# Kernel tuning notes

Measured on AMD Instinct MI355X. Metric: run time of the kernel, lower is better.

Reference implementation:

```python
import jax, jax.numpy as jnp
import numpy as np

B = 16384      # batch
T = 14         # number of embedding tables
L = 100000     # rows per table (table has L+1 rows due to the +1 offset)
E = 16         # em_size
H = 50         # user click history length


def setup_inputs() -> dict:
    key = jax.random.key(0)
    ks = jax.random.split(key, 10)
    sparse_features = jax.random.randint(ks[0], (B, T), 0, L, dtype=jnp.int32)
    dense_features = jax.random.normal(ks[1], (B, 1), dtype=jnp.float32)
    user_click_history = jax.random.randint(ks[2], (B, H), 0, L, dtype=jnp.int32)
    # stacked EmbeddingBag weights: [T, L+1, E]
    W = jax.random.normal(ks[3], (T, L + 1, E), dtype=jnp.float32) * 0.01
    fc1_w = jax.random.normal(ks[4], (200, 241), dtype=jnp.float32) / np.sqrt(241).astype(np.float32)
    fc1_b = jnp.zeros((200,), jnp.float32)
    fc2_w = jax.random.normal(ks[5], (80, 200), dtype=jnp.float32) / np.sqrt(200).astype(np.float32)
    fc2_b = jnp.zeros((80,), jnp.float32)
    fc3_w = jax.random.normal(ks[6], (2, 80), dtype=jnp.float32) / np.sqrt(80).astype(np.float32)
    fc3_b = jnp.zeros((2,), jnp.float32)
    return dict(sparse_features=sparse_features, dense_features=dense_features,
                user_click_history=user_click_history, W=W,
                fc1_w=fc1_w, fc1_b=fc1_b, fc2_w=fc2_w, fc2_b=fc2_b,
                fc3_w=fc3_w, fc3_b=fc3_b)


def reference(sparse_features, dense_features, user_click_history, W,
              fc1_w, fc1_b, fc2_w, fc2_b, fc3_w, fc3_b):
    # Per-table single-index EmbeddingBag(sum) == plain lookup. Batched gather
    # across all T tables at once: [B, T, E]
    embs = W[jnp.arange(T)[None, :], sparse_features + 1]
    embs = embs.reshape(embs.shape[0], T * E)  # [B, T*E]
    # tables[0].weight row 0 is zeroed before the history lookup (padding row).
    W0 = W[0].at[0].set(0.0)
    hist = W0[user_click_history + 1].sum(axis=1)  # [B, E] EmbeddingBag sum
    x = jnp.concatenate([embs, hist, dense_features], axis=1)  # [B, 241]
    x = jax.nn.relu(x @ fc1_w.T + fc1_b)
    x = jax.nn.relu(x @ fc2_w.T + fc2_b)
    return x @ fc3_w.T + fc3_b  # [B, 2]
```

## Files before the change

kernel.cpp:

```cpp
#include <hip/hip_runtime.h>


using u16 = unsigned short;
typedef __attribute__((ext_vector_type(8))) short short8v;
typedef __attribute__((ext_vector_type(4))) short short4v;
typedef __attribute__((ext_vector_type(4))) float floatx4;

constexpr int W1_ELEMS = 13 * 8 * 64 * 8;
constexpr int W2_ELEMS = 5 * 7 * 64 * 8;

__device__ __forceinline__ u16 f2bf(float f) {
  unsigned u = __float_as_uint(f);
  unsigned r = (u + 0x7fffu + ((u >> 16) & 1u)) >> 16;
  return (u16)r;
}
__device__ __forceinline__ float bf2f(u16 h) {
  return __uint_as_float(((unsigned)h) << 16);
}

__global__ void build_frags(const float* __restrict__ w1, const float* __restrict__ w2,
                            u16* __restrict__ w1h, u16* __restrict__ w2h) {
  int tid = blockIdx.x * blockDim.x + threadIdx.x;
  if (tid < 13 * 8 * 64) {
    int l = tid & 63;
    int g = tid >> 6;
    int kt = g & 7, nt = g >> 3;
    int n = nt * 16 + (l & 15);
    int kb = kt * 32 + (l >> 4) * 8;
    short8v h8;
#pragma unroll
    for (int e = 0; e < 8; ++e) {
      int k = kb + e;
      float v = (n < 200 && k < 241) ? w1[n * 241 + k] : 0.f;
      h8[e] = (short)f2bf(v);
    }
    *(short8v*)&w1h[tid * 8] = h8;
  } else if (tid < 13 * 8 * 64 + 5 * 7 * 64) {
    int t2 = tid - 13 * 8 * 64;
    int l = t2 & 63;
    int g = t2 >> 6;
    int kt = g % 7, nt = g / 7;
    int n = nt * 16 + (l & 15);
    int kb = kt * 32 + (l >> 4) * 8;
    short8v h8;
#pragma unroll
    for (int e = 0; e < 8; ++e) {
      int k = kb + e;
      float v = (k < 200) ? w2[n * 200 + k] : 0.f;
      h8[e] = (short)f2bf(v);
    }
    *(short8v*)&w2h[t2 * 8] = h8;
  }
}

__global__ __launch_bounds__(256, 4) void fused_kernel(
    const int* __restrict__ sf, const float* __restrict__ dense,
    const int* __restrict__ hist, const float* __restrict__ W,
    const u16* __restrict__ w1h, const u16* __restrict__ w2h,
    const float* __restrict__ b1, const float* __restrict__ b2,
    const float* __restrict__ w3, const float* __restrict__ b3,
    float* __restrict__ out) {
  __shared__ u16 A1h[8 * 64 * 8], A1l[8 * 64 * 8];
  __shared__ u16 A2h[7 * 64 * 8], A2l[7 * 64 * 8];
  __shared__ float o2[16 * 84];

  const int tid = threadIdx.x;
  const int l = tid & 63;
  const int wv = tid >> 6;
  const int row0 = blockIdx.x * 16;
  short8v z8 = {0, 0, 0, 0, 0, 0, 0, 0};

  const int ntbase = (wv == 0) ? 0 : 4 + 3 * (wv - 1);
  const int ntcnt = (wv == 0) ? 4 : 3;

  short8v bhr[2][4];
#pragma unroll
  for (int kk = 0; kk < 2; ++kk)
#pragma unroll
    for (int i = 0; i < 4; ++i)
      bhr[kk][i] = (i < ntcnt) ? *(const short8v*)&w1h[(((ntbase + i) * 8 + kk) * 64 + l) * 8]
                               : z8;

#pragma unroll
  for (int it = 0; it < 4; ++it) {
    int g = tid + it * 256;
    if (g < 896) {
      int q = g & 3, rt = g >> 2;
      int r = rt & 15, t = rt >> 4;
      int idx = sf[(row0 + r) * 14 + t] + 1;
      const float* p = W + ((size_t)t * 100001 + (size_t)idx) * 16 + q * 4;
      int k0 = t * 16 + q * 4;
      int kt = k0 >> 5, kg = (k0 >> 3) & 3, e0 = k0 & 7;
      short4v h4, l4;
#pragma unroll
      for (int d = 0; d < 4; ++d) {
        float v = p[d];
        u16 hi = f2bf(v);
        h4[d] = (short)hi;
        l4[d] = (short)f2bf(v - bf2f(hi));
      }
      int base = (kt * 64 + kg * 16 + r) * 8 + e0;
      *(short4v*)&A1h[base] = h4;
      *(short4v*)&A1l[base] = l4;
    }
  }

  {
    int r = tid >> 4, rem = tid & 15, q = rem & 3, s = rem >> 2;
    const int* hp = hist + (row0 + r) * 50;
    const float* Wq = W + q * 4;
    float a0 = 0.f, a1 = 0.f, a2 = 0.f, a3 = 0.f;
#pragma unroll
    for (int hh = 0; hh < 12; ++hh) {
      int idx = hp[s + hh * 4] + 1;
      const float* p = Wq + (size_t)idx * 16;
      a0 += p[0];
      a1 += p[1];
      a2 += p[2];
      a3 += p[3];
    }
    if (s < 2) {
      int idx = hp[48 + s] + 1;
      const float* p = Wq + (size_t)idx * 16;
      a0 += p[0];
      a1 += p[1];
      a2 += p[2];
      a3 += p[3];
    }
    a0 += __shfl_xor(a0, 4);
    a1 += __shfl_xor(a1, 4);
    a2 += __shfl_xor(a2, 4);
    a3 += __shfl_xor(a3, 4);
    a0 += __shfl_xor(a0, 8);
    a1 += __shfl_xor(a1, 8);
    a2 += __shfl_xor(a2, 8);
    a3 += __shfl_xor(a3, 8);
    if (s == 0) {
      float vals[4] = {a0, a1, a2, a3};
      short4v h4, l4;
#pragma unroll
      for (int d = 0; d < 4; ++d) {
        u16 hi = f2bf(vals[d]);
        h4[d] = (short)hi;
        l4[d] = (short)f2bf(vals[d] - bf2f(hi));
      }
      int base = (7 * 64 + (q >> 1) * 16 + r) * 8 + ((q * 4) & 7);
      *(short4v*)&A1h[base] = h4;
      *(short4v*)&A1l[base] = l4;
      if (q == 0) {
        float dv = dense[row0 + r];
        u16 dh = f2bf(dv), dl = f2bf(dv - bf2f(dh));
        short8v dh8 = z8, dl8 = z8;
        dh8[0] = (short)dh;
        dl8[0] = (short)dl;
        *(short8v*)&A1h[(7 * 64 + 32 + r) * 8] = dh8;
        *(short8v*)&A1l[(7 * 64 + 32 + r) * 8] = dl8;
        *(short8v*)&A1h[(7 * 64 + 48 + r) * 8] = z8;
        *(short8v*)&A1l[(7 * 64 + 48 + r) * 8] = z8;
      }
    }
  }
  __syncthreads();

  floatx4 acc[4];
#pragma unroll
  for (int i = 0; i < 4; ++i) acc[i] = (floatx4){0.f, 0.f, 0.f, 0.f};

#pragma unroll
  for (int kt = 0; kt < 8; ++kt) {
    short8v ah = *(const short8v*)&A1h[(kt * 64 + l) * 8];
    short8v al = *(const short8v*)&A1l[(kt * 64 + l) * 8];
#pragma unroll
    for (int i = 0; i < 4; ++i) {
      if (i < ntcnt) {
        short8v cb = bhr[kt & 1][i];
        if (kt < 6) bhr[kt & 1][i] = *(const short8v*)&w1h[(((ntbase + i) * 8 + kt + 2) * 64 + l) * 8];
        acc[i] = __builtin_amdgcn_mfma_f32_16x16x32_bf16(ah, cb, acc[i], 0, 0, 0);
        acc[i] = __builtin_amdgcn_mfma_f32_16x16x32_bf16(al, cb, acc[i], 0, 0, 0);
      }
    }
  }

  const int ntA = wv;
  short8v bra[2], brb[2];
  bra[0] = *(const short8v*)&w2h[((ntA * 7 + 0) * 64 + l) * 8];
  bra[1] = *(const short8v*)&w2h[((ntA * 7 + 1) * 64 + l) * 8];
  if (wv == 0) {
    brb[0] = *(const short8v*)&w2h[((4 * 7 + 0) * 64 + l) * 8];
    brb[1] = *(const short8v*)&w2h[((4 * 7 + 1) * 64 + l) * 8];
  } else {
    brb[0] = z8;
    brb[1] = z8;
  }

#pragma unroll
  for (int i = 0; i < 4; ++i) {
    if (i < ntcnt) {
      int n = (ntbase + i) * 16 + (l & 15);
      float bias = (n < 200) ? b1[n] : 0.f;
#pragma unroll
      for (int g = 0; g < 4; ++g) {
        float v = (n < 200) ? fmaxf(acc[i][g] + bias, 0.f) : 0.f;
        int m = (l >> 4) * 4 + g;
        u16 hi = f2bf(v), lo = f2bf(v - bf2f(hi));
        int kt2 = n >> 5, kg2 = (n >> 3) & 3, e = n & 7;
        int pos = (kt2 * 64 + kg2 * 16 + m) * 8 + e;
        A2h[pos] = hi;
        A2l[pos] = lo;
      }
    }
  }
  if (wv == 1 && l < 32) {
    *(short8v*)&A2h[(6 * 64 + 32 + l) * 8] = z8;
    *(short8v*)&A2l[(6 * 64 + 32 + l) * 8] = z8;
  }
  __syncthreads();

  floatx4 acca = (floatx4){0.f, 0.f, 0.f, 0.f};
  floatx4 accb = (floatx4){0.f, 0.f, 0.f, 0.f};
#pragma unroll
  for (int kt = 0; kt < 7; ++kt) {
    short8v ah = *(const short8v*)&A2h[(kt * 64 + l) * 8];
    short8v al = *(const short8v*)&A2l[(kt * 64 + l) * 8];
    short8v ca = bra[kt & 1];
    if (kt < 5) bra[kt & 1] = *(const short8v*)&w2h[((ntA * 7 + kt + 2) * 64 + l) * 8];
    acca = __builtin_amdgcn_mfma_f32_16x16x32_bf16(ah, ca, acca, 0, 0, 0);
    acca = __builtin_amdgcn_mfma_f32_16x16x32_bf16(al, ca, acca, 0, 0, 0);
    if (wv == 0) {
      short8v cb = brb[kt & 1];
      if (kt < 5) brb[kt & 1] = *(const short8v*)&w2h[((4 * 7 + kt + 2) * 64 + l) * 8];
      accb = __builtin_amdgcn_mfma_f32_16x16x32_bf16(ah, cb, accb, 0, 0, 0);
      accb = __builtin_amdgcn_mfma_f32_16x16x32_bf16(al, cb, accb, 0, 0, 0);
    }
  }

  {
    int n = ntA * 16 + (l & 15);
    float bias = b2[n];
#pragma unroll
    for (int g = 0; g < 4; ++g) {
      int r = (l >> 4) * 4 + g;
      o2[r * 84 + n] = fmaxf(acca[g] + bias, 0.f);
    }
    if (wv == 0) {
      int n2 = 64 + (l & 15);
      float bias2 = b2[n2];
#pragma unroll
      for (int g = 0; g < 4; ++g) {
        int r = (l >> 4) * 4 + g;
        o2[r * 84 + n2] = fmaxf(accb[g] + bias2, 0.f);
      }
    }
  }
  __syncthreads();

  if (tid < 32) {
    int r = tid >> 1, o = tid & 1;
    float a = b3[o];
    const float* orow = &o2[r * 84];
    const float* wrow = &w3[o * 80];
#pragma unroll
    for (int j = 0; j < 80; j += 4) {
      floatx4 xv = *(const floatx4*)&orow[j];
      floatx4 wv4 = *(const floatx4*)&wrow[j];
      a += xv[0] * wv4[0] + xv[1] * wv4[1] + xv[2] * wv4[2] + xv[3] * wv4[3];
    }
    out[(row0 + r) * 2 + o] = a;
  }
}

extern "C" void kernel_launch(void* const* d_in, const int* in_sizes, int n_in,
                              void* d_out, int out_size, void* d_ws, size_t ws_size,
                              hipStream_t stream) {
  const int* sf = (const int*)d_in[0];
  const float* dense = (const float*)d_in[1];
  const int* hist = (const int*)d_in[2];
  const float* W = (const float*)d_in[3];
  const float* w1 = (const float*)d_in[4];
  const float* b1 = (const float*)d_in[5];
  const float* w2 = (const float*)d_in[6];
  const float* b2 = (const float*)d_in[7];
  const float* w3 = (const float*)d_in[8];
  const float* b3 = (const float*)d_in[9];
  float* out = (float*)d_out;

  u16* w1h = (u16*)d_ws;
  u16* w2h = w1h + W1_ELEMS;

  build_frags<<<dim3(35), dim3(256), 0, stream>>>(w1, w2, w1h, w2h);
  fused_kernel<<<dim3(1024), dim3(256), 0, stream>>>(sf, dense, hist, W, w1h, w2h,
                                                     b1, b2, w3, b3, out);
}
```

Before: 31.08 us.

## Convert table 0 to bf16 for history gather and drop low-part MFMAs for embeddings

Adds a precompute pass that converts all of table 0 to bf16 each call. The history EmbeddingBag then gathers half-size bf16 rows, using 8 lanes per row with 16-byte loads. The 14 sparse embeddings are now rounded to a single bf16 and keep no low-part residual, so the hi/lo split MFMA runs only for the history/dense tile. This halves the MFMA count for layer 1 and shrinks shared memory. The trade-offs are extra per-call conversion traffic over a 6.4MB table and reduced precision in both embedding paths. Note that table 0 row 0 is not zeroed, though the before code had the same issue.

```diff
diff --git a/kernel.cpp b/kernel.cpp
--- a/kernel.cpp
+++ b/kernel.cpp
@@ -8,6 +8,8 @@
 
 constexpr int W1_ELEMS = 13 * 8 * 64 * 8;
 constexpr int W2_ELEMS = 5 * 7 * 64 * 8;
+constexpr int W0_ROWS = 100001;
+constexpr int W0_ELEMS = W0_ROWS * 16;
 
 __device__ __forceinline__ u16 f2bf(float f) {
   unsigned u = __float_as_uint(f);
@@ -18,49 +20,73 @@
   return __uint_as_float(((unsigned)h) << 16);
 }
 
-__global__ void build_frags(const float* __restrict__ w1, const float* __restrict__ w2,
-                            u16* __restrict__ w1h, u16* __restrict__ w2h) {
-  int tid = blockIdx.x * blockDim.x + threadIdx.x;
-  if (tid < 13 * 8 * 64) {
-    int l = tid & 63;
-    int g = tid >> 6;
-    int kt = g & 7, nt = g >> 3;
-    int n = nt * 16 + (l & 15);
-    int kb = kt * 32 + (l >> 4) * 8;
-    short8v h8;
-#pragma unroll
-    for (int e = 0; e < 8; ++e) {
-      int k = kb + e;
-      float v = (n < 200 && k < 241) ? w1[n * 241 + k] : 0.f;
-      h8[e] = (short)f2bf(v);
-    }
-    *(short8v*)&w1h[tid * 8] = h8;
-  } else if (tid < 13 * 8 * 64 + 5 * 7 * 64) {
-    int t2 = tid - 13 * 8 * 64;
-    int l = t2 & 63;
-    int g = t2 >> 6;
-    int kt = g % 7, nt = g / 7;
-    int n = nt * 16 + (l & 15);
-    int kb = kt * 32 + (l >> 4) * 8;
-    short8v h8;
-#pragma unroll
-    for (int e = 0; e < 8; ++e) {
-      int k = kb + e;
-      float v = (k < 200) ? w2[n * 200 + k] : 0.f;
-      h8[e] = (short)f2bf(v);
-    }
-    *(short8v*)&w2h[t2 * 8] = h8;
+__global__ void precompute(const float* __restrict__ w1, const float* __restrict__ w2,
+                           const float* __restrict__ W,
+                           u16* __restrict__ w1h, u16* __restrict__ w2h,
+                           u16* __restrict__ w0b) {
+  int b = blockIdx.x;
+  if (b < 35) {
+    int tid = b * 256 + threadIdx.x;
+    if (tid < 13 * 8 * 64) {
+      int l = tid & 63;
+      int g = tid >> 6;
+      int kt = g & 7, nt = g >> 3;
+      int n = nt * 16 + (l & 15);
+      int kb = kt * 32 + (l >> 4) * 8;
+      short8v h8;
+#pragma unroll
+      for (int e = 0; e < 8; ++e) {
+        int k = kb + e;
+        float v = (n < 200 && k < 241) ? w1[n * 241 + k] : 0.f;
+        h8[e] = (short)f2bf(v);
+      }
+      *(short8v*)&w1h[tid * 8] = h8;
+    } else if (tid < 13 * 8 * 64 + 5 * 7 * 64) {
+      int t2 = tid - 13 * 8 * 64;
+      int l = t2 & 63;
+      int g = t2 >> 6;
+      int kt = g % 7, nt = g / 7;
+      int n = nt * 16 + (l & 15);
+      int kb = kt * 32 + (l >> 4) * 8;
+      short8v h8;
+#pragma unroll
+      for (int e = 0; e < 8; ++e) {
+        int k = kb + e;
+        float v = (k < 200) ? w2[n * 200 + k] : 0.f;
+        h8[e] = (short)f2bf(v);
+      }
+      *(short8v*)&w2h[t2 * 8] = h8;
+    }
+  } else {
+    int t = (b - 35) * 256 + threadIdx.x;
+    int base = t * 8;
+    if (base < W0_ELEMS) {
+      floatx4 f0 = *(const floatx4*)(W + base);
+      floatx4 f1 = *(const floatx4*)(W + base + 4);
+      short8v o;
+      o[0] = (short)f2bf(f0[0]);
+      o[1] = (short)f2bf(f0[1]);
+      o[2] = (short)f2bf(f0[2]);
+      o[3] = (short)f2bf(f0[3]);
+      o[4] = (short)f2bf(f1[0]);
+      o[5] = (short)f2bf(f1[1]);
+      o[6] = (short)f2bf(f1[2]);
+      o[7] = (short)f2bf(f1[3]);
+      *(short8v*)(w0b + base) = o;
+    }
   }
 }
 
 __global__ __launch_bounds__(256, 4) void fused_kernel(
     const int* __restrict__ sf, const float* __restrict__ dense,
     const int* __restrict__ hist, const float* __restrict__ W,
+    const u16* __restrict__ w0b,
     const u16* __restrict__ w1h, const u16* __restrict__ w2h,
     const float* __restrict__ b1, const float* __restrict__ b2,
     const float* __restrict__ w3, const float* __restrict__ b3,
     float* __restrict__ out) {
-  __shared__ u16 A1h[8 * 64 * 8], A1l[8 * 64 * 8];
+  __shared__ u16 A1h[8 * 64 * 8];
+  __shared__ u16 A1l7[64 * 8];
   __shared__ u16 A2h[7 * 64 * 8], A2l[7 * 64 * 8];
   __shared__ float o2[16 * 84];
 
@@ -88,65 +114,50 @@
       int q = g & 3, rt = g >> 2;
       int r = rt & 15, t = rt >> 4;
       int idx = sf[(row0 + r) * 14 + t] + 1;
-      const float* p = W + ((size_t)t * 100001 + (size_t)idx) * 16 + q * 4;
+      const floatx4 v4 = *(const floatx4*)(W + ((size_t)t * 100001 + (size_t)idx) * 16 + q * 4);
       int k0 = t * 16 + q * 4;
       int kt = k0 >> 5, kg = (k0 >> 3) & 3, e0 = k0 & 7;
-      short4v h4, l4;
-#pragma unroll
-      for (int d = 0; d < 4; ++d) {
-        float v = p[d];
-        u16 hi = f2bf(v);
-        h4[d] = (short)hi;
-        l4[d] = (short)f2bf(v - bf2f(hi));
-      }
-      int base = (kt * 64 + kg * 16 + r) * 8 + e0;
-      *(short4v*)&A1h[base] = h4;
-      *(short4v*)&A1l[base] = l4;
+      short4v h4;
+#pragma unroll
+      for (int d = 0; d < 4; ++d) h4[d] = (short)f2bf(v4[d]);
+      *(short4v*)&A1h[(kt * 64 + kg * 16 + r) * 8 + e0] = h4;
     }
   }
 
   {
-    int r = tid >> 4, rem = tid & 15, q = rem & 3, s = rem >> 2;
+    int r = tid >> 4, rem = tid & 15, q = rem & 1, s = rem >> 1;
     const int* hp = hist + (row0 + r) * 50;
-    const float* Wq = W + q * 4;
-    float a0 = 0.f, a1 = 0.f, a2 = 0.f, a3 = 0.f;
-#pragma unroll
-    for (int hh = 0; hh < 12; ++hh) {
-      int idx = hp[s + hh * 4] + 1;
-      const float* p = Wq + (size_t)idx * 16;
-      a0 += p[0];
-      a1 += p[1];
-      a2 += p[2];
-      a3 += p[3];
+    const u16* Wq = w0b + q * 8;
+    float a[8] = {0.f, 0.f, 0.f, 0.f, 0.f, 0.f, 0.f, 0.f};
+#pragma unroll
+    for (int hh = 0; hh < 6; ++hh) {
+      int idx = hp[s + hh * 8] + 1;
+      short8v v = *(const short8v*)(Wq + (size_t)idx * 16);
+#pragma unroll
+      for (int d = 0; d < 8; ++d) a[d] += bf2f((u16)v[d]);
     }
     if (s < 2) {
       int idx = hp[48 + s] + 1;
-      const float* p = Wq + (size_t)idx * 16;
-      a0 += p[0];
-      a1 += p[1];
-      a2 += p[2];
-      a3 += p[3];
-    }
-    a0 += __shfl_xor(a0, 4);
-    a1 += __shfl_xor(a1, 4);
-    a2 += __shfl_xor(a2, 4);
-    a3 += __shfl_xor(a3, 4);
-    a0 += __shfl_xor(a0, 8);
-    a1 += __shfl_xor(a1, 8);
-    a2 += __shfl_xor(a2, 8);
-    a3 += __shfl_xor(a3, 8);
+      short8v v = *(const short8v*)(Wq + (size_t)idx * 16);
+#pragma unroll
+      for (int d = 0; d < 8; ++d) a[d] += bf2f((u16)v[d]);
+    }
+#pragma unroll
+    for (int d = 0; d < 8; ++d) {
+      a[d] += __shfl_xor(a[d], 2);
+      a[d] += __shfl_xor(a[d], 4);
+      a[d] += __shfl_xor(a[d], 8);
+    }
     if (s == 0) {
-      float vals[4] = {a0, a1, a2, a3};
-      short4v h4, l4;
-#pragma unroll
-      for (int d = 0; d < 4; ++d) {
-        u16 hi = f2bf(vals[d]);
-        h4[d] = (short)hi;
-        l4[d] = (short)f2bf(vals[d] - bf2f(hi));
-      }
-      int base = (7 * 64 + (q >> 1) * 16 + r) * 8 + ((q * 4) & 7);
-      *(short4v*)&A1h[base] = h4;
-      *(short4v*)&A1l[base] = l4;
+      short8v h8, l8;
+#pragma unroll
+      for (int d = 0; d < 8; ++d) {
+        u16 hi = f2bf(a[d]);
+        h8[d] = (short)hi;
+        l8[d] = (short)f2bf(a[d] - bf2f(hi));
+      }
+      *(short8v*)&A1h[(7 * 64 + q * 16 + r) * 8] = h8;
+      *(short8v*)&A1l7[(q * 16 + r) * 8] = l8;
       if (q == 0) {
         float dv = dense[row0 + r];
         u16 dh = f2bf(dv), dl = f2bf(dv - bf2f(dh));
@@ -154,9 +165,9 @@
         dh8[0] = (short)dh;
         dl8[0] = (short)dl;
         *(short8v*)&A1h[(7 * 64 + 32 + r) * 8] = dh8;
-        *(short8v*)&A1l[(7 * 64 + 32 + r) * 8] = dl8;
+        *(short8v*)&A1l7[(32 + r) * 8] = dl8;
         *(short8v*)&A1h[(7 * 64 + 48 + r) * 8] = z8;
-        *(short8v*)&A1l[(7 * 64 + 48 + r) * 8] = z8;
+        *(short8v*)&A1l7[(48 + r) * 8] = z8;
       }
     }
   }
@@ -169,14 +180,15 @@
 #pragma unroll
   for (int kt = 0; kt < 8; ++kt) {
     short8v ah = *(const short8v*)&A1h[(kt * 64 + l) * 8];
-    short8v al = *(const short8v*)&A1l[(kt * 64 + l) * 8];
+    short8v al7;
+    if (kt == 7) al7 = *(const short8v*)&A1l7[l * 8];
 #pragma unroll
     for (int i = 0; i < 4; ++i) {
       if (i < ntcnt) {
         short8v cb = bhr[kt & 1][i];
         if (kt < 6) bhr[kt & 1][i] = *(const short8v*)&w1h[(((ntbase + i) * 8 + kt + 2) * 64 + l) * 8];
         acc[i] = __builtin_amdgcn_mfma_f32_16x16x32_bf16(ah, cb, acc[i], 0, 0, 0);
-        acc[i] = __builtin_amdgcn_mfma_f32_16x16x32_bf16(al, cb, acc[i], 0, 0, 0);
+        if (kt == 7) acc[i] = __builtin_amdgcn_mfma_f32_16x16x32_bf16(al7, cb, acc[i], 0, 0, 0);
       }
     }
   }
@@ -286,8 +298,10 @@
 
   u16* w1h = (u16*)d_ws;
   u16* w2h = w1h + W1_ELEMS;
-
-  build_frags<<<dim3(35), dim3(256), 0, stream>>>(w1, w2, w1h, w2h);
-  fused_kernel<<<dim3(1024), dim3(256), 0, stream>>>(sf, dense, hist, W, w1h, w2h,
+  u16* w0b = w2h + W2_ELEMS;
+
+  int conv_blocks = (W0_ELEMS / 8 + 255) / 256;
+  precompute<<<dim3(35 + conv_blocks), dim3(256), 0, stream>>>(w1, w2, W, w1h, w2h, w0b);
+  fused_kernel<<<dim3(1024), dim3(256), 0, stream>>>(sf, dense, hist, W, w0b, w1h, w2h,
                                                      b1, b2, w3, b3, out);
 }
```

Result: faster. 30.28 us (-2.6%).

## Split gathers into a prep kernel and run MLP on 64-row tiles

Applied to the files above, without the earlier changes.

The embedding gathers and history sums move into a separate prep kernel that writes MFMA-ready bf16 fragments to workspace, merged with the weight-fragment build. The MLP kernel then handles 64 rows per block instead of 16, so each weight fragment loaded from global is reused across four row subtiles. The table embeddings now use a single bf16 (hi only) instead of the hi/lo split, which halves the first-layer MFMAs but lowers precision. The cost is an extra global round trip for the activations and far fewer MLP blocks (256), which may leave CUs underused.

```diff
diff --git a/kernel.cpp b/kernel.cpp
--- a/kernel.cpp
+++ b/kernel.cpp
@@ -8,6 +8,8 @@
 
 constexpr int W1_ELEMS = 13 * 8 * 64 * 8;
 constexpr int W2_ELEMS = 5 * 7 * 64 * 8;
+constexpr int EF_ELEMS = 1024 * 7 * 64 * 8;
+constexpr int HS_ELEMS = 1024 * 1024;
 
 __device__ __forceinline__ u16 f2bf(float f) {
   unsigned u = __float_as_uint(f);
@@ -18,102 +20,72 @@
   return __uint_as_float(((unsigned)h) << 16);
 }
 
-__global__ void build_frags(const float* __restrict__ w1, const float* __restrict__ w2,
-                            u16* __restrict__ w1h, u16* __restrict__ w2h) {
-  int tid = blockIdx.x * blockDim.x + threadIdx.x;
-  if (tid < 13 * 8 * 64) {
-    int l = tid & 63;
-    int g = tid >> 6;
-    int kt = g & 7, nt = g >> 3;
-    int n = nt * 16 + (l & 15);
-    int kb = kt * 32 + (l >> 4) * 8;
-    short8v h8;
-#pragma unroll
-    for (int e = 0; e < 8; ++e) {
-      int k = kb + e;
-      float v = (n < 200 && k < 241) ? w1[n * 241 + k] : 0.f;
-      h8[e] = (short)f2bf(v);
-    }
-    *(short8v*)&w1h[tid * 8] = h8;
-  } else if (tid < 13 * 8 * 64 + 5 * 7 * 64) {
-    int t2 = tid - 13 * 8 * 64;
-    int l = t2 & 63;
-    int g = t2 >> 6;
-    int kt = g % 7, nt = g / 7;
-    int n = nt * 16 + (l & 15);
-    int kb = kt * 32 + (l >> 4) * 8;
-    short8v h8;
-#pragma unroll
-    for (int e = 0; e < 8; ++e) {
-      int k = kb + e;
-      float v = (k < 200) ? w2[n * 200 + k] : 0.f;
-      h8[e] = (short)f2bf(v);
-    }
-    *(short8v*)&w2h[t2 * 8] = h8;
-  }
-}
-
-__global__ __launch_bounds__(256, 4) void fused_kernel(
-    const int* __restrict__ sf, const float* __restrict__ dense,
-    const int* __restrict__ hist, const float* __restrict__ W,
-    const u16* __restrict__ w1h, const u16* __restrict__ w2h,
-    const float* __restrict__ b1, const float* __restrict__ b2,
-    const float* __restrict__ w3, const float* __restrict__ b3,
-    float* __restrict__ out) {
-  __shared__ u16 A1h[8 * 64 * 8], A1l[8 * 64 * 8];
-  __shared__ u16 A2h[7 * 64 * 8], A2l[7 * 64 * 8];
-  __shared__ float o2[16 * 84];
-
-  const int tid = threadIdx.x;
-  const int l = tid & 63;
-  const int wv = tid >> 6;
-  const int row0 = blockIdx.x * 16;
+__global__ __launch_bounds__(256) void prep_kernel(
+    const float* __restrict__ w1, const float* __restrict__ w2,
+    const float* __restrict__ W, const int* __restrict__ sf,
+    const int* __restrict__ hist, const float* __restrict__ dense,
+    u16* __restrict__ w1h, u16* __restrict__ w2h,
+    u16* __restrict__ ef, u16* __restrict__ hs) {
+  const int b = blockIdx.x;
+  const int tix = threadIdx.x;
   short8v z8 = {0, 0, 0, 0, 0, 0, 0, 0};
 
-  const int ntbase = (wv == 0) ? 0 : 4 + 3 * (wv - 1);
-  const int ntcnt = (wv == 0) ? 4 : 3;
-
-  short8v bhr[2][4];
-#pragma unroll
-  for (int kk = 0; kk < 2; ++kk)
-#pragma unroll
-    for (int i = 0; i < 4; ++i)
-      bhr[kk][i] = (i < ntcnt) ? *(const short8v*)&w1h[(((ntbase + i) * 8 + kk) * 64 + l) * 8]
-                               : z8;
-
-#pragma unroll
-  for (int it = 0; it < 4; ++it) {
-    int g = tid + it * 256;
-    if (g < 896) {
-      int q = g & 3, rt = g >> 2;
-      int r = rt & 15, t = rt >> 4;
-      int idx = sf[(row0 + r) * 14 + t] + 1;
-      const float* p = W + ((size_t)t * 100001 + (size_t)idx) * 16 + q * 4;
-      int k0 = t * 16 + q * 4;
-      int kt = k0 >> 5, kg = (k0 >> 3) & 3, e0 = k0 & 7;
-      short4v h4, l4;
-#pragma unroll
-      for (int d = 0; d < 4; ++d) {
-        float v = p[d];
-        u16 hi = f2bf(v);
-        h4[d] = (short)hi;
-        l4[d] = (short)f2bf(v - bf2f(hi));
-      }
-      int base = (kt * 64 + kg * 16 + r) * 8 + e0;
-      *(short4v*)&A1h[base] = h4;
-      *(short4v*)&A1l[base] = l4;
-    }
-  }
-
-  {
-    int r = tid >> 4, rem = tid & 15, q = rem & 3, s = rem >> 2;
+  if (b < 35) {
+    int tid = b * 256 + tix;
+    if (tid < 13 * 8 * 64) {
+      int l = tid & 63;
+      int g = tid >> 6;
+      int kt = g & 7, nt = g >> 3;
+      int n = nt * 16 + (l & 15);
+      int kb = kt * 32 + (l >> 4) * 8;
+      short8v h8;
+#pragma unroll
+      for (int e = 0; e < 8; ++e) {
+        int k = kb + e;
+        float v = (n < 200 && k < 241) ? w1[n * 241 + k] : 0.f;
+        h8[e] = (short)f2bf(v);
+      }
+      *(short8v*)&w1h[tid * 8] = h8;
+    } else if (tid < 13 * 8 * 64 + 5 * 7 * 64) {
+      int t2 = tid - 13 * 8 * 64;
+      int l = t2 & 63;
+      int g = t2 >> 6;
+      int kt = g % 7, nt = g / 7;
+      int n = nt * 16 + (l & 15);
+      int kb = kt * 32 + (l >> 4) * 8;
+      short8v h8;
+#pragma unroll
+      for (int e = 0; e < 8; ++e) {
+        int k = kb + e;
+        float v = (k < 200) ? w2[n * 200 + k] : 0.f;
+        h8[e] = (short)f2bf(v);
+      }
+      *(short8v*)&w2h[t2 * 8] = h8;
+    }
+  } else if (b < 3619) {
+    int g = (b - 35) * 256 + tix;
+    int t = g >> 16;
+    int bb = (g >> 2) & 16383;
+    int q = g & 3;
+    int idx = sf[bb * 14 + t] + 1;
+    floatx4 v4 = *(const floatx4*)(W + ((size_t)t * 100001 + (size_t)idx) * 16 + q * 4);
+    short4v h4;
+#pragma unroll
+    for (int d = 0; d < 4; ++d) h4[d] = (short)f2bf(v4[d]);
+    int k0 = t * 16 + q * 4;
+    int kt = k0 >> 5, kg = (k0 >> 3) & 3, e0 = k0 & 7;
+    int tile = bb >> 4, r = bb & 15;
+    *(short4v*)&ef[((tile * 7 + kt) * 64 + kg * 16 + r) * 8 + e0] = h4;
+  } else {
+    int tile = b - 3619;
+    int row0 = tile * 16;
+    int r = tix >> 4, rem = tix & 15, q = rem & 3, s = rem >> 2;
     const int* hp = hist + (row0 + r) * 50;
-    const float* Wq = W + q * 4;
     float a0 = 0.f, a1 = 0.f, a2 = 0.f, a3 = 0.f;
 #pragma unroll
     for (int hh = 0; hh < 12; ++hh) {
       int idx = hp[s + hh * 4] + 1;
-      const float* p = Wq + (size_t)idx * 16;
+      floatx4 p = *(const floatx4*)(W + (size_t)idx * 16 + q * 4);
       a0 += p[0];
       a1 += p[1];
       a2 += p[2];
@@ -121,7 +93,7 @@
     }
     if (s < 2) {
       int idx = hp[48 + s] + 1;
-      const float* p = Wq + (size_t)idx * 16;
+      floatx4 p = *(const floatx4*)(W + (size_t)idx * 16 + q * 4);
       a0 += p[0];
       a1 += p[1];
       a2 += p[2];
@@ -144,93 +116,156 @@
         h4[d] = (short)hi;
         l4[d] = (short)f2bf(vals[d] - bf2f(hi));
       }
-      int base = (7 * 64 + (q >> 1) * 16 + r) * 8 + ((q * 4) & 7);
-      *(short4v*)&A1h[base] = h4;
-      *(short4v*)&A1l[base] = l4;
+      u16* ht = hs + (size_t)tile * 1024;
+      int base = ((q >> 1) * 16 + r) * 8 + ((q * 4) & 7);
+      *(short4v*)&ht[base] = h4;
+      *(short4v*)&ht[512 + base] = l4;
       if (q == 0) {
         float dv = dense[row0 + r];
         u16 dh = f2bf(dv), dl = f2bf(dv - bf2f(dh));
         short8v dh8 = z8, dl8 = z8;
         dh8[0] = (short)dh;
         dl8[0] = (short)dl;
-        *(short8v*)&A1h[(7 * 64 + 32 + r) * 8] = dh8;
-        *(short8v*)&A1l[(7 * 64 + 32 + r) * 8] = dl8;
-        *(short8v*)&A1h[(7 * 64 + 48 + r) * 8] = z8;
-        *(short8v*)&A1l[(7 * 64 + 48 + r) * 8] = z8;
-      }
-    }
-  }
-  __syncthreads();
-
-  floatx4 acc[4];
-#pragma unroll
-  for (int i = 0; i < 4; ++i) acc[i] = (floatx4){0.f, 0.f, 0.f, 0.f};
+        *(short8v*)&ht[(32 + r) * 8] = dh8;
+        *(short8v*)&ht[512 + (32 + r) * 8] = dl8;
+        *(short8v*)&ht[(48 + r) * 8] = z8;
+        *(short8v*)&ht[512 + (48 + r) * 8] = z8;
+      }
+    }
+  }
+}
+
+__global__ __launch_bounds__(256, 1) void mlp_kernel(
+    const u16* __restrict__ ef, const u16* __restrict__ hs,
+    const u16* __restrict__ w1h, const u16* __restrict__ w2h,
+    const float* __restrict__ b1, const float* __restrict__ b2,
+    const float* __restrict__ w3, const float* __restrict__ b3,
+    float* __restrict__ out) {
+  __shared__ u16 A2h[4 * 7 * 64 * 8], A2l[4 * 7 * 64 * 8];
+  __shared__ float o2[64 * 84];
+
+  const int tid = threadIdx.x;
+  const int l = tid & 63;
+  const int wv = tid >> 6;
+  const int blk = blockIdx.x;
+  const int row0 = blk * 64;
+  short8v z8 = {0, 0, 0, 0, 0, 0, 0, 0};
+  const int ntbase = (wv == 0) ? 0 : 4 + 3 * (wv - 1);
+  const int ntcnt = (wv == 0) ? 4 : 3;
+
+  short8v a7h[4], a7l[4];
+#pragma unroll
+  for (int sub = 0; sub < 4; ++sub) {
+    const u16* ht = hs + (size_t)(blk * 4 + sub) * 1024;
+    a7h[sub] = *(const short8v*)&ht[l * 8];
+    a7l[sub] = *(const short8v*)&ht[512 + l * 8];
+  }
+  short8v ga[2][4];
+#pragma unroll
+  for (int kk = 0; kk < 2; ++kk)
+#pragma unroll
+    for (int sub = 0; sub < 4; ++sub)
+      ga[kk][sub] = *(const short8v*)&ef[(((blk * 4 + sub) * 7 + kk) * 64 + l) * 8];
+  short8v bhr[2][4];
+#pragma unroll
+  for (int kk = 0; kk < 2; ++kk)
+#pragma unroll
+    for (int i = 0; i < 4; ++i)
+      bhr[kk][i] = (i < ntcnt) ? *(const short8v*)&w1h[(((ntbase + i) * 8 + kk) * 64 + l) * 8]
+                               : z8;
+
+  floatx4 acc[4][4];
+#pragma unroll
+  for (int i = 0; i < 4; ++i)
+#pragma unroll
+    for (int sub = 0; sub < 4; ++sub) acc[i][sub] = (floatx4){0.f, 0.f, 0.f, 0.f};
 
 #pragma unroll
   for (int kt = 0; kt < 8; ++kt) {
-    short8v ah = *(const short8v*)&A1h[(kt * 64 + l) * 8];
-    short8v al = *(const short8v*)&A1l[(kt * 64 + l) * 8];
+    const int cur = kt & 1;
+    short8v a_[4];
+#pragma unroll
+    for (int sub = 0; sub < 4; ++sub) a_[sub] = (kt < 7) ? ga[cur][sub] : a7h[sub];
+    if (kt < 5) {
+#pragma unroll
+      for (int sub = 0; sub < 4; ++sub)
+        ga[cur][sub] = *(const short8v*)&ef[(((blk * 4 + sub) * 7 + kt + 2) * 64 + l) * 8];
+    }
 #pragma unroll
     for (int i = 0; i < 4; ++i) {
       if (i < ntcnt) {
-        short8v cb = bhr[kt & 1][i];
-        if (kt < 6) bhr[kt & 1][i] = *(const short8v*)&w1h[(((ntbase + i) * 8 + kt + 2) * 64 + l) * 8];
-        acc[i] = __builtin_amdgcn_mfma_f32_16x16x32_bf16(ah, cb, acc[i], 0, 0, 0);
-        acc[i] = __builtin_amdgcn_mfma_f32_16x16x32_bf16(al, cb, acc[i], 0, 0, 0);
+        short8v cb = bhr[cur][i];
+        if (kt < 6)
+          bhr[cur][i] = *(const short8v*)&w1h[(((ntbase + i) * 8 + kt + 2) * 64 + l) * 8];
+#pragma unroll
+        for (int sub = 0; sub < 4; ++sub) {
+          acc[i][sub] = __builtin_amdgcn_mfma_f32_16x16x32_bf16(a_[sub], cb, acc[i][sub], 0, 0, 0);
+          if (kt == 7)
+            acc[i][sub] = __builtin_amdgcn_mfma_f32_16x16x32_bf16(a7l[sub], cb, acc[i][sub], 0, 0, 0);
+        }
       }
     }
   }
 
   const int ntA = wv;
+  const bool dual = (wv == 1);
   short8v bra[2], brb[2];
   bra[0] = *(const short8v*)&w2h[((ntA * 7 + 0) * 64 + l) * 8];
   bra[1] = *(const short8v*)&w2h[((ntA * 7 + 1) * 64 + l) * 8];
-  if (wv == 0) {
-    brb[0] = *(const short8v*)&w2h[((4 * 7 + 0) * 64 + l) * 8];
-    brb[1] = *(const short8v*)&w2h[((4 * 7 + 1) * 64 + l) * 8];
-  } else {
-    brb[0] = z8;
-    brb[1] = z8;
-  }
+  brb[0] = dual ? *(const short8v*)&w2h[((4 * 7 + 0) * 64 + l) * 8] : z8;
+  brb[1] = dual ? *(const short8v*)&w2h[((4 * 7 + 1) * 64 + l) * 8] : z8;
 
 #pragma unroll
   for (int i = 0; i < 4; ++i) {
     if (i < ntcnt) {
       int n = (ntbase + i) * 16 + (l & 15);
       float bias = (n < 200) ? b1[n] : 0.f;
-#pragma unroll
-      for (int g = 0; g < 4; ++g) {
-        float v = (n < 200) ? fmaxf(acc[i][g] + bias, 0.f) : 0.f;
-        int m = (l >> 4) * 4 + g;
-        u16 hi = f2bf(v), lo = f2bf(v - bf2f(hi));
-        int kt2 = n >> 5, kg2 = (n >> 3) & 3, e = n & 7;
-        int pos = (kt2 * 64 + kg2 * 16 + m) * 8 + e;
-        A2h[pos] = hi;
-        A2l[pos] = lo;
+      int kt2 = n >> 5, kg2 = (n >> 3) & 3, e = n & 7;
+#pragma unroll
+      for (int sub = 0; sub < 4; ++sub) {
+#pragma unroll
+        for (int g = 0; g < 4; ++g) {
+          float v = (n < 200) ? fmaxf(acc[i][sub][g] + bias, 0.f) : 0.f;
+          int m = (l >> 4) * 4 + g;
+          u16 hi = f2bf(v), lo = f2bf(v - bf2f(hi));
+          int pos = ((sub * 7 + kt2) * 64 + kg2 * 16 + m) * 8 + e;
+          A2h[pos] = hi;
+          A2l[pos] = lo;
+        }
       }
     }
   }
   if (wv == 1 && l < 32) {
-    *(short8v*)&A2h[(6 * 64 + 32 + l) * 8] = z8;
-    *(short8v*)&A2l[(6 * 64 + 32 + l) * 8] = z8;
+#pragma unroll
+    for (int sub = 0; sub < 4; ++sub) {
+      *(short8v*)&A2h[((sub * 7 + 6) * 64 + 32 + l) * 8] = z8;
+      *(short8v*)&A2l[((sub * 7 + 6) * 64 + 32 + l) * 8] = z8;
+    }
   }
   __syncthreads();
 
-  floatx4 acca = (floatx4){0.f, 0.f, 0.f, 0.f};
-  floatx4 accb = (floatx4){0.f, 0.f, 0.f, 0.f};
+  floatx4 acc2a[4], acc2b[4];
+#pragma unroll
+  for (int sub = 0; sub < 4; ++sub) {
+    acc2a[sub] = (floatx4){0.f, 0.f, 0.f, 0.f};
+    acc2b[sub] = (floatx4){0.f, 0.f, 0.f, 0.f};
+  }
 #pragma unroll
   for (int kt = 0; kt < 7; ++kt) {
-    short8v ah = *(const short8v*)&A2h[(kt * 64 + l) * 8];
-    short8v al = *(const short8v*)&A2l[(kt * 64 + l) * 8];
     short8v ca = bra[kt & 1];
     if (kt < 5) bra[kt & 1] = *(const short8v*)&w2h[((ntA * 7 + kt + 2) * 64 + l) * 8];
-    acca = __builtin_amdgcn_mfma_f32_16x16x32_bf16(ah, ca, acca, 0, 0, 0);
-    acca = __builtin_amdgcn_mfma_f32_16x16x32_bf16(al, ca, acca, 0, 0, 0);
-    if (wv == 0) {
-      short8v cb = brb[kt & 1];
-      if (kt < 5) brb[kt & 1] = *(const short8v*)&w2h[((4 * 7 + kt + 2) * 64 + l) * 8];
-      accb = __builtin_amdgcn_mfma_f32_16x16x32_bf16(ah, cb, accb, 0, 0, 0);
-      accb = __builtin_amdgcn_mfma_f32_16x16x32_bf16(al, cb, accb, 0, 0, 0);
+    short8v cb2 = brb[kt & 1];
+    if (dual && kt < 5) brb[kt & 1] = *(const short8v*)&w2h[((4 * 7 + kt + 2) * 64 + l) * 8];
+#pragma unroll
+    for (int sub = 0; sub < 4; ++sub) {
+      short8v ah = *(const short8v*)&A2h[((sub * 7 + kt) * 64 + l) * 8];
+      short8v al = *(const short8v*)&A2l[((sub * 7 + kt) * 64 + l) * 8];
+      acc2a[sub] = __builtin_amdgcn_mfma_f32_16x16x32_bf16(ah, ca, acc2a[sub], 0, 0, 0);
+      acc2a[sub] = __builtin_amdgcn_mfma_f32_16x16x32_bf16(al, ca, acc2a[sub], 0, 0, 0);
+      if (dual) {
+        acc2b[sub] = __builtin_amdgcn_mfma_f32_16x16x32_bf16(ah, cb2, acc2b[sub], 0, 0, 0);
+        acc2b[sub] = __builtin_amdgcn_mfma_f32_16x16x32_bf16(al, cb2, acc2b[sub], 0, 0, 0);
+      }
     }
   }
 
@@ -238,23 +273,27 @@
     int n = ntA * 16 + (l & 15);
     float bias = b2[n];
 #pragma unroll
-    for (int g = 0; g < 4; ++g) {
-      int r = (l >> 4) * 4 + g;
-      o2[r * 84 + n] = fmaxf(acca[g] + bias, 0.f);
-    }
-    if (wv == 0) {
+    for (int sub = 0; sub < 4; ++sub)
+#pragma unroll
+      for (int g = 0; g < 4; ++g) {
+        int r2 = sub * 16 + (l >> 4) * 4 + g;
+        o2[r2 * 84 + n] = fmaxf(acc2a[sub][g] + bias, 0.f);
+      }
+    if (dual) {
       int n2 = 64 + (l & 15);
       float bias2 = b2[n2];
 #pragma unroll
-      for (int g = 0; g < 4; ++g) {
-        int r = (l >> 4) * 4 + g;
-        o2[r * 84 + n2] = fmaxf(accb[g] + bias2, 0.f);
-      }
+      for (int sub = 0; sub < 4; ++sub)
+#pragma unroll
+        for (int g = 0; g < 4; ++g) {
+          int r2 = sub * 16 + (l >> 4) * 4 + g;
+          o2[r2 * 84 + n2] = fmaxf(acc2b[sub][g] + bias2, 0.f);
+        }
     }
   }
   __syncthreads();
 
-  if (tid < 32) {
+  if (tid < 128) {
     int r = tid >> 1, o = tid & 1;
     float a = b3[o];
     const float* orow = &o2[r * 84];
@@ -286,8 +325,10 @@
 
   u16* w1h = (u16*)d_ws;
   u16* w2h = w1h + W1_ELEMS;
-
-  build_frags<<<dim3(35), dim3(256), 0, stream>>>(w1, w2, w1h, w2h);
-  fused_kernel<<<dim3(1024), dim3(256), 0, stream>>>(sf, dense, hist, W, w1h, w2h,
-                                                     b1, b2, w3, b3, out);
-}
+  u16* ef = w2h + W2_ELEMS;
+  u16* hs = ef + EF_ELEMS;
+
+  prep_kernel<<<dim3(35 + 3584 + 1024), dim3(256), 0, stream>>>(
+      w1, w2, W, sf, hist, dense, w1h, w2h, ef, hs);
+  mlp_kernel<<<dim3(256), dim3(256), 0, stream>>>(ef, hs, w1h, w2h, b1, b2, w3, b3, out);
+}
```

New measurement: 37.02 us. 19.1% more time.
